# Optimization experiments

Hardware: AMD Instinct MI355X
Metric: run time of the kernel (lower is better)

## Reference

```python
import jax, jax.numpy as jnp
import numpy as np

def setup_inputs() -> dict:
    key = jax.random.key(0)
    k1, k2, k3 = jax.random.split(key, 3)
    B, N, D = 4, 2048, 1024
    x = jax.random.normal(k1, (B, N, D), dtype=jnp.float32)
    # nn.Linear weights are (out_features, in_features); init scale ~1/sqrt(D)
    W_Q = jax.random.normal(k2, (D, D), dtype=jnp.float32) / np.sqrt(D)
    W_K = jax.random.normal(k3, (D, D), dtype=jnp.float32) / np.sqrt(D)
    return {"x": x, "W_Q": W_Q, "W_K": W_K, "n_iters": 5}

def reference(x, W_Q, W_K, n_iters):
    # K = Linear(W_K)(x) = x @ W_K.T  -> (B, N, D)
    K = jnp.einsum('bnd,kd->bnk', x, W_K)
    y = x
    for _ in range(n_iters):
        Q = jnp.einsum('bnd,kd->bnk', y, W_Q)          # (B, N, D)
        scores = jnp.einsum('bnd,bmd->bnm', K, Q)       # K @ Q^T, (B, N, N)
        probs = jax.nn.softmax(scores, axis=-1)
        y = jnp.einsum('bnm,bmd->bnd', probs, x)        # (B, N, D)
    return y
```

## Files before the change

### kernel.cpp

```cpp
#include <hip/hip_runtime.h>
#include <cstdint>

typedef _Float16 f16;
typedef __attribute__((ext_vector_type(8))) _Float16 v8h;
typedef __attribute__((ext_vector_type(4))) float v4f;

#define LO_SCALE 4096.0f
#define LO_INV   2.44140625e-4f

__device__ __forceinline__ void split2(float f, f16& h, f16& l) {
    h = (f16)f;
    l = (f16)((f - (float)h) * LO_SCALE);
}

__device__ __forceinline__ void gload_lds16(const void* g, void* l) {
    __builtin_amdgcn_global_load_lds(
        (const __attribute__((address_space(1))) unsigned int*)(uintptr_t)g,
        (__attribute__((address_space(3))) unsigned int*)(unsigned int)(uintptr_t)l,
        16, 0, 0);
}

__global__ __launch_bounds__(256)
void gemm_nt_2limb(const f16* __restrict__ A1, const f16* __restrict__ A2,
                   const f16* __restrict__ B1, const f16* __restrict__ B2,
                   float* __restrict__ C32, f16* __restrict__ Ch,
                   f16* __restrict__ Cl, int mode, int N, int K)
{
    __shared__ f16 lds[4 * 128 * 32];
    f16* lA1 = lds;
    f16* lA2 = lds + 128 * 32;
    f16* lB1 = lds + 2 * 128 * 32;
    f16* lB2 = lds + 3 * 128 * 32;

    const int tid  = threadIdx.x;
    const int lane = tid & 63;
    const int wave = tid >> 6;
    const int wm = wave >> 1, wn = wave & 1;
    const int fr = lane & 15, quad = lane >> 4;
    const int row0 = blockIdx.y * 128;
    const int col0 = blockIdx.x * 128;
    const int l4 = lane >> 2;
    const int c8 = (lane & 3) * 8;

    v4f accB[4][4], accS[4][4];
#pragma unroll
    for (int i = 0; i < 4; ++i)
#pragma unroll
        for (int j = 0; j < 4; ++j) {
            accB[i][j] = {0.f, 0.f, 0.f, 0.f};
            accS[i][j] = {0.f, 0.f, 0.f, 0.f};
        }

    for (int k0 = 0; k0 < K; k0 += 32) {
#pragma unroll
        for (int t = 0; t < 2; ++t) {
            const int slot = wave + 4 * t;
            const int r = slot * 16 + l4;
            const size_t ga = (size_t)(row0 + r) * K + (k0 + c8);
            const size_t gb = (size_t)(col0 + r) * K + (k0 + c8);
            const unsigned loff = slot * 1024;
            gload_lds16(A1 + ga, (char*)lA1 + loff);
            gload_lds16(A2 + ga, (char*)lA2 + loff);
            gload_lds16(B1 + gb, (char*)lB1 + loff);
            gload_lds16(B2 + gb, (char*)lB2 + loff);
        }
        __syncthreads();

        v8h a1[4], a2[4], b1[4], b2[4];
#pragma unroll
        for (int i = 0; i < 4; ++i) {
            const int off = (wm * 64 + i * 16 + fr) * 32 + quad * 8;
            a1[i] = *(const v8h*)&lA1[off];
            a2[i] = *(const v8h*)&lA2[off];
        }
#pragma unroll
        for (int j = 0; j < 4; ++j) {
            const int off = (wn * 64 + j * 16 + fr) * 32 + quad * 8;
            b1[j] = *(const v8h*)&lB1[off];
            b2[j] = *(const v8h*)&lB2[off];
        }
#pragma unroll
        for (int i = 0; i < 4; ++i)
#pragma unroll
            for (int j = 0; j < 4; ++j) {
                accB[i][j] = __builtin_amdgcn_mfma_f32_16x16x32_f16(a1[i], b1[j], accB[i][j], 0, 0, 0);
                accS[i][j] = __builtin_amdgcn_mfma_f32_16x16x32_f16(a2[i], b1[j], accS[i][j], 0, 0, 0);
                accS[i][j] = __builtin_amdgcn_mfma_f32_16x16x32_f16(a1[i], b2[j], accS[i][j], 0, 0, 0);
            }
        __syncthreads();
    }

#pragma unroll
    for (int i = 0; i < 4; ++i)
#pragma unroll
        for (int j = 0; j < 4; ++j) {
            const int row = row0 + wm * 64 + i * 16 + quad * 4;
            const int col = col0 + wn * 64 + j * 16 + fr;
#pragma unroll
            for (int r = 0; r < 4; ++r) {
                const float v = accB[i][j][r] + accS[i][j][r] * LO_INV;
                const size_t off = (size_t)(row + r) * N + col;
                if (mode == 0) {
                    C32[off] = v;
                } else if (mode == 1) {
                    f16 h, l; split2(v, h, l);
                    Ch[off] = h; Cl[off] = l;
                } else {
                    C32[off] = v;
                    Ch[off] = (f16)v;
                }
            }
        }
}

__global__ __launch_bounds__(512)
void gemm_nt_2limb_256(const f16* __restrict__ A1, const f16* __restrict__ A2,
                       const f16* __restrict__ B1, const f16* __restrict__ B2,
                       float* __restrict__ C32, f16* __restrict__ Ch,
                       int N, int K)
{
    __shared__ f16 lds[2 * 24576];

    const int bid = blockIdx.x;
    const int lid = (bid & 7) * 32 + (bid >> 3);
    const int col0 = (lid & 7) * 128;
    const int row0 = (lid >> 3) * 256;

    const int tid  = threadIdx.x;
    const int lane = tid & 63;
    const int wave = tid >> 6;
    const int wm = wave >> 1;
    const int wn = wave & 1;
    const int fr = lane & 15, quad = lane >> 4;
    const int NT = K >> 5;

    const int trow = tid >> 2;
    const int tchunk = tid & 3;

    auto STAGE = [&](int T) {
        const unsigned bufB = (unsigned)(T & 1) * 49152u;
        const int k0 = T * 32;
#pragma unroll
        for (int rd = 0; rd < 2; ++rd) {
            const int r = trow + rd * 128;
            const int sc = (tchunk ^ ((r >> 1) & 3)) * 8;
            const size_t ga = (size_t)(row0 + r) * K + k0 + sc;
            const unsigned dof = (unsigned)(rd * 8192 + wave * 1024);
            gload_lds16(A1 + ga, (char*)lds + bufB + dof);
            gload_lds16(A2 + ga, (char*)lds + bufB + 16384u + dof);
        }
        {
            const int r = trow;
            const int sc = (tchunk ^ ((r >> 1) & 3)) * 8;
            const size_t gb = (size_t)(col0 + r) * K + k0 + sc;
            const unsigned dof = (unsigned)(wave * 1024);
            gload_lds16(B1 + gb, (char*)lds + bufB + 32768u + dof);
            gload_lds16(B2 + gb, (char*)lds + bufB + 40960u + dof);
        }
    };

    auto LRD = [&](const f16* base, int row) {
        return *(const v8h*)&base[row * 32 + ((quad ^ ((row >> 1) & 3)) * 8)];
    };

    v4f accB[4][4], accS[4][4];
#pragma unroll
    for (int i = 0; i < 4; ++i)
#pragma unroll
        for (int j = 0; j < 4; ++j) {
            accB[i][j] = {0.f, 0.f, 0.f, 0.f};
            accS[i][j] = {0.f, 0.f, 0.f, 0.f};
        }

    STAGE(0);
    asm volatile("s_waitcnt vmcnt(0)" ::: "memory");
    __builtin_amdgcn_s_barrier();

    for (int t = 0; t < NT; ++t) {
        const int bc = (t & 1) * 24576;
        const f16* lA1 = lds + bc;
        const f16* lA2 = lds + bc + 8192;
        const f16* lB1 = lds + bc + 16384;
        const f16* lB2 = lds + bc + 20480;

        v8h b1[4], b2[4];
#pragma unroll
        for (int j = 0; j < 4; ++j) {
            b1[j] = LRD(lB1, wn * 64 + j * 16 + fr);
            b2[j] = LRD(lB2, wn * 64 + j * 16 + fr);
        }
        {
            v8h a1 = LRD(lA1, wm * 64 + 0 + fr);
            v8h a2 = LRD(lA2, wm * 64 + 0 + fr);
            if (t + 1 < NT) STAGE(t + 1);
            __builtin_amdgcn_s_barrier();
            asm volatile("s_waitcnt lgkmcnt(0)" ::: "memory");
            __builtin_amdgcn_s_setprio(1);
#pragma unroll
            for (int j = 0; j < 4; ++j) {
                accB[0][j] = __builtin_amdgcn_mfma_f32_16x16x32_f16(a1, b1[j], accB[0][j], 0, 0, 0);
                accS[0][j] = __builtin_amdgcn_mfma_f32_16x16x32_f16(a2, b1[j], accS[0][j], 0, 0, 0);
                accS[0][j] = __builtin_amdgcn_mfma_f32_16x16x32_f16(a1, b2[j], accS[0][j], 0, 0, 0);
            }
            __builtin_amdgcn_s_setprio(0);
            __builtin_amdgcn_s_barrier();
        }

#pragma unroll
        for (int p = 1; p < 4; ++p) {
            v8h a1 = LRD(lA1, wm * 64 + p * 16 + fr);
            v8h a2 = LRD(lA2, wm * 64 + p * 16 + fr);
            __builtin_amdgcn_s_barrier();
            asm volatile("s_waitcnt lgkmcnt(0)" ::: "memory");
            __builtin_amdgcn_s_setprio(1);
#pragma unroll
            for (int j = 0; j < 4; ++j) {
                accB[p][j] = __builtin_amdgcn_mfma_f32_16x16x32_f16(a1, b1[j], accB[p][j], 0, 0, 0);
                accS[p][j] = __builtin_amdgcn_mfma_f32_16x16x32_f16(a2, b1[j], accS[p][j], 0, 0, 0);
                accS[p][j] = __builtin_amdgcn_mfma_f32_16x16x32_f16(a1, b2[j], accS[p][j], 0, 0, 0);
            }
            __builtin_amdgcn_s_setprio(0);
            if (p == 3)
                asm volatile("s_waitcnt vmcnt(0)" ::: "memory");
            __builtin_amdgcn_s_barrier();
        }
    }

#pragma unroll
    for (int i = 0; i < 4; ++i)
#pragma unroll
        for (int j = 0; j < 4; ++j) {
            const int row = row0 + wm * 64 + i * 16 + quad * 4;
            const int col = col0 + wn * 64 + j * 16 + fr;
#pragma unroll
            for (int r = 0; r < 4; ++r) {
                const float v = accB[i][j][r] + accS[i][j][r] * LO_INV;
                const size_t off = (size_t)(row + r) * N + col;
                C32[off] = v;
                Ch[off] = (f16)v;
            }
        }
}

__global__ __launch_bounds__(512)
void gemm_nt_f16_256(const f16* __restrict__ A, const f16* __restrict__ B,
                     f16* __restrict__ C, int N, int K,
                     size_t sA, size_t sB, size_t sC)
{
    __shared__ f16 lds[2 * 2 * 256 * 64];

    const int bz = blockIdx.z;
    A += (size_t)bz * sA; B += (size_t)bz * sB; C += (size_t)bz * sC;

    const int tid  = threadIdx.x;
    const int lane = tid & 63;
    const int wave = tid >> 6;
    const int wm = wave >> 2;
    const int wn = wave & 3;
    const int fr = lane & 15, quad = lane >> 4;
    const int row0 = blockIdx.y * 256;
    const int col0 = blockIdx.x * 256;
    const int NT = K >> 6;

    const int rsub = tid >> 3;
    const int csub = (((tid & 7) ^ ((tid >> 3) & 7)) * 8);

    auto STAGE = [&](int T) {
        const unsigned bufB = (unsigned)(T & 1) * 65536u;
#pragma unroll
        for (int q = 0; q < 4; ++q) {
            const f16* op = (q >= 2) ? B : A;
            const int r0 = ((q >= 2) ? col0 : row0) + (q & 1) * 128;
#pragma unroll
            for (int t2 = 0; t2 < 2; ++t2) {
                const f16* g = op + (size_t)(r0 + t2 * 64 + rsub) * K + T * 64 + csub;
                gload_lds16(g, (char*)lds + bufB + (unsigned)(q >> 1) * 32768u
                                 + (unsigned)(q & 1) * 16384u
                                 + (unsigned)(t2 * 8192 + wave * 1024));
            }
        }
    };

    auto LRD = [&](const f16* base, int row, int ks) {
        return *(const v8h*)&base[row * 64 + (((ks * 4 + quad) ^ (row & 7)) * 8)];
    };

    v4f acc[8][4];
#pragma unroll
    for (int i = 0; i < 8; ++i)
#pragma unroll
        for (int j = 0; j < 4; ++j)
            acc[i][j] = {0.f, 0.f, 0.f, 0.f};

    STAGE(0);
    asm volatile("s_waitcnt vmcnt(0)" ::: "memory");
    __builtin_amdgcn_s_barrier();

    for (int t = 0; t < NT; ++t) {
        const int bc = (t & 1) * 32768;
        const f16* lA = lds + bc;
        const f16* lB = lds + bc + 16384;

        v8h bfr[4][2];
#pragma unroll
        for (int j = 0; j < 4; ++j)
#pragma unroll
            for (int ks = 0; ks < 2; ++ks)
                bfr[j][ks] = LRD(lB, wn * 64 + j * 16 + fr, ks);
        {
            v8h a0[2], a1[2];
#pragma unroll
            for (int ks = 0; ks < 2; ++ks) {
                a0[ks] = LRD(lA, wm * 128 + 0 + fr, ks);
                a1[ks] = LRD(lA, wm * 128 + 16 + fr, ks);
            }
            if (t + 1 < NT) STAGE(t + 1);
            __builtin_amdgcn_s_barrier();
            asm volatile("s_waitcnt lgkmcnt(0)" ::: "memory");
            __builtin_amdgcn_s_setprio(1);
#pragma unroll
            for (int j = 0; j < 4; ++j) {
                acc[0][j] = __builtin_amdgcn_mfma_f32_16x16x32_f16(a0[0], bfr[j][0], acc[0][j], 0, 0, 0);
                acc[0][j] = __builtin_amdgcn_mfma_f32_16x16x32_f16(a0[1], bfr[j][1], acc[0][j], 0, 0, 0);
                acc[1][j] = __builtin_amdgcn_mfma_f32_16x16x32_f16(a1[0], bfr[j][0], acc[1][j], 0, 0, 0);
                acc[1][j] = __builtin_amdgcn_mfma_f32_16x16x32_f16(a1[1], bfr[j][1], acc[1][j], 0, 0, 0);
            }
            __builtin_amdgcn_s_setprio(0);
            __builtin_amdgcn_s_barrier();
        }

#pragma unroll
        for (int p = 1; p < 4; ++p) {
            v8h ap[2][2];
#pragma unroll
            for (int u = 0; u < 2; ++u)
#pragma unroll
                for (int ks = 0; ks < 2; ++ks)
                    ap[u][ks] = LRD(lA, wm * 128 + (p * 2 + u) * 16 + fr, ks);
            __builtin_amdgcn_s_barrier();
            asm volatile("s_waitcnt lgkmcnt(0)" ::: "memory");
            __builtin_amdgcn_s_setprio(1);
#pragma unroll
            for (int u = 0; u < 2; ++u)
#pragma unroll
                for (int j = 0; j < 4; ++j) {
                    acc[p * 2 + u][j] = __builtin_amdgcn_mfma_f32_16x16x32_f16(ap[u][0], bfr[j][0], acc[p * 2 + u][j], 0, 0, 0);
                    acc[p * 2 + u][j] = __builtin_amdgcn_mfma_f32_16x16x32_f16(ap[u][1], bfr[j][1], acc[p * 2 + u][j], 0, 0, 0);
                }
            __builtin_amdgcn_s_setprio(0);
            if (p == 3)
                asm volatile("s_waitcnt vmcnt(0)" ::: "memory");
            __builtin_amdgcn_s_barrier();
        }
    }

#pragma unroll
    for (int i = 0; i < 8; ++i)
#pragma unroll
        for (int j = 0; j < 4; ++j) {
            const int row = row0 + wm * 128 + i * 16 + quad * 4;
            const int col = col0 + wn * 64 + j * 16 + fr;
#pragma unroll
            for (int r = 0; r < 4; ++r)
                C[(size_t)(row + r) * N + col] = (f16)acc[i][j][r];
        }
}

__global__ __launch_bounds__(256)
void split_f32(const float* __restrict__ in, f16* __restrict__ h,
               f16* __restrict__ l, int n)
{
    const int i = (blockIdx.x * 256 + threadIdx.x) * 4;
    if (i >= n) return;
    const float4 v = *(const float4*)(in + i);
    f16 hh[4], ll[4];
    split2(v.x, hh[0], ll[0]);
    split2(v.y, hh[1], ll[1]);
    split2(v.z, hh[2], ll[2]);
    split2(v.w, hh[3], ll[3]);
    *(ushort4*)(h + i) = *(const ushort4*)hh;
    *(ushort4*)(l + i) = *(const ushort4*)ll;
}

__global__ __launch_bounds__(256)
void transpose_split(const float* __restrict__ in, f16* __restrict__ oh,
                     f16* __restrict__ ol, int R, int C)
{
    __shared__ float tile[32][33];
    const int tx = threadIdx.x & 31, ty = threadIdx.x >> 5;
    const int ic = blockIdx.x * 32 + tx;
    const int ir = blockIdx.y * 32 + ty;
#pragma unroll
    for (int k = 0; k < 32; k += 8)
        tile[ty + k][tx] = in[(size_t)(ir + k) * C + ic];
    __syncthreads();
    const int oc  = blockIdx.y * 32 + tx;
    const int orr = blockIdx.x * 32 + ty;
#pragma unroll
    for (int k = 0; k < 32; k += 8) {
        f16 h, l;
        split2(tile[tx][ty + k], h, l);
        oh[(size_t)(orr + k) * R + oc] = h;
        ol[(size_t)(orr + k) * R + oc] = l;
    }
}

#define CAP 1024

__global__ __launch_bounds__(256)
void refine_pv(const f16* __restrict__ S, const float* __restrict__ Kt,
               const float* __restrict__ Y, const float* __restrict__ X,
               float* __restrict__ Yout, f16* __restrict__ Yh)
{
    const int r = blockIdx.x;
    const int b = r >> 11;
    const int t = threadIdx.x;
    const int wave = t >> 6, lane = t & 63;

    __shared__ float red[4];
    __shared__ int cnt;
    __shared__ int idxs[CAP + 8];
    __shared__ float ex[CAP + 8];

    float s[8];
    {
        const v8h sv = *(const v8h*)(S + (size_t)r * 2048 + t * 8);
#pragma unroll
        for (int k = 0; k < 8; ++k) s[k] = (float)sv[k];
    }
    float m = s[0];
#pragma unroll
    for (int k = 1; k < 8; ++k) m = fmaxf(m, s[k]);
#pragma unroll
    for (int off = 32; off > 0; off >>= 1) m = fmaxf(m, __shfl_xor(m, off));
    if (lane == 0) red[wave] = m;
    if (t == 0) cnt = 0;
    __syncthreads();
    m = fmaxf(fmaxf(red[0], red[1]), fmaxf(red[2], red[3]));

    const float thresh = m - 18.0f;
#pragma unroll
    for (int k = 0; k < 8; ++k)
        if (s[k] > thresh) {
            const int p = atomicAdd(&cnt, 1);
            if (p < CAP) idxs[p] = t * 8 + k;
        }
    __syncthreads();
    const int count = min(cnt, CAP);

    const float* krow  = Kt + (size_t)r * 1024;
    const float* ybase = Y + (size_t)b * 2048 * 1024;
    for (int j = wave; j < count; j += 4) {
        const float* yrow = ybase + (size_t)idxs[j] * 1024;
        float acc = 0.f;
#pragma unroll
        for (int d = 0; d < 4; ++d) {
            const int e = lane * 4 + d * 256;
            const float4 kv = *(const float4*)(krow + e);
            const float4 yv = *(const float4*)(yrow + e);
            acc += kv.x * yv.x + kv.y * yv.y + kv.z * yv.z + kv.w * yv.w;
        }
#pragma unroll
        for (int off = 32; off > 0; off >>= 1) acc += __shfl_xor(acc, off);
        if (lane == 0) ex[j] = acc;
    }
    __syncthreads();

    float lm = -3.0e38f;
    for (int j = t; j < count; j += 256) lm = fmaxf(lm, ex[j]);
#pragma unroll
    for (int off = 32; off > 0; off >>= 1) lm = fmaxf(lm, __shfl_xor(lm, off));
    if (lane == 0) red[wave] = lm;
    __syncthreads();
    const float M2 = fmaxf(fmaxf(red[0], red[1]), fmaxf(red[2], red[3]));
    __syncthreads();

    float ls = 0.f;
    for (int j = t; j < count; j += 256) {
        const float e = expf(ex[j] - M2);
        ex[j] = e;
        ls += e;
    }
#pragma unroll
    for (int off = 32; off > 0; off >>= 1) ls += __shfl_xor(ls, off);
    if (lane == 0) red[wave] = ls;
    __syncthreads();
    const float inv = 1.0f / (red[0] + red[1] + red[2] + red[3]);
    for (int j = t; j < count; j += 256) ex[j] *= inv;
    const int countPad = (count + 7) & ~7;
    if (t < countPad - count) {
        ex[count + t]   = 0.f;
        idxs[count + t] = 0;
    }
    __syncthreads();

    const float* xb = X + (size_t)b * 2048 * 1024;
    float4 acc = {0.f, 0.f, 0.f, 0.f};
    for (int j = 0; j < countPad; j += 8) {
        float4 v[8];
        float  pw[8];
#pragma unroll
        for (int k = 0; k < 8; ++k) {
            pw[k] = ex[j + k];
            v[k] = *(const float4*)(xb + (size_t)idxs[j + k] * 1024 + t * 4);
        }
#pragma unroll
        for (int k = 0; k < 8; ++k) {
            acc.x += pw[k] * v[k].x;
            acc.y += pw[k] * v[k].y;
            acc.z += pw[k] * v[k].z;
            acc.w += pw[k] * v[k].w;
        }
    }
    const size_t o = (size_t)r * 1024 + t * 4;
    *(float4*)(Yout + o) = acc;
    f16 h[4] = {(f16)acc.x, (f16)acc.y, (f16)acc.z, (f16)acc.w};
    *(ushort4*)(Yh + o) = *(const ushort4*)h;
}

extern "C" void kernel_launch(void* const* d_in, const int* in_sizes, int n_in,
                              void* d_out, int out_size, void* d_ws, size_t ws_size,
                              hipStream_t stream)
{
    const float* x  = (const float*)d_in[0];
    const float* Wq = (const float*)d_in[1];
    const float* Wk = (const float*)d_in[2];
    const int n_iters = 5;

    const size_t NXe = 8388608;
    const size_t NWe = 1048576;
    const size_t NSe = 16777216;
    const size_t NR  = 8192;

    char* p = (char*)d_ws;
    f16* xh   = (f16*)p; p += NXe * 2;
    f16* xl   = (f16*)p; p += NXe * 2;
    f16* wkth = (f16*)p; p += NWe * 2;
    f16* wktl = (f16*)p; p += NWe * 2;
    f16* wqth = (f16*)p; p += NWe * 2;
    f16* wqtl = (f16*)p; p += NWe * 2;
    f16* vth  = (f16*)p; p += NWe * 2;
    f16* vtl  = (f16*)p; p += NWe * 2;
    float* kt32 = (float*)p; p += NXe * 4;
    f16*  kt16  = (f16*)p;  p += NXe * 2;
    f16*  st    = (f16*)p;  p += NSe * 2;
    f16*  yh    = (f16*)p;  p += NXe * 2;
    float* y1   = (float*)p; p += NXe * 4;
    float* y2   = (float*)p; p += NXe * 4;
    if ((size_t)(p - (char*)d_ws) > ws_size) return;

    float* out = (float*)d_out;

    split_f32<<<dim3(NXe / 1024), dim3(256), 0, stream>>>(x, xh, xl, (int)NXe);
    transpose_split<<<dim3(32, 32), dim3(256), 0, stream>>>(Wk, wkth, wktl, 1024, 1024);
    transpose_split<<<dim3(32, 32), dim3(256), 0, stream>>>(Wq, wqth, wqtl, 1024, 1024);
    gemm_nt_2limb<<<dim3(8, 8), dim3(256), 0, stream>>>(
        wqth, wqtl, wkth, wktl, nullptr, vth, vtl, 1, 1024, 1024);
    gemm_nt_2limb_256<<<dim3(256), dim3(512), 0, stream>>>(
        xh, xl, vth, vtl, kt32, kt16, 1024, 1024);

    const float* yr = x;
    float* pingpong[2] = {y1, y2};
    for (int it = 0; it < n_iters; ++it) {
        float* yw = (it == n_iters - 1) ? out : pingpong[it & 1];
        const f16* Bop = (it == 0) ? xh : yh;
        gemm_nt_f16_256<<<dim3(8, 8, 4), dim3(512), 0, stream>>>(
            kt16, Bop, st, 2048, 1024,
            (size_t)2048 * 1024, (size_t)2048 * 1024, (size_t)2048 * 2048);
        refine_pv<<<dim3(NR), dim3(256), 0, stream>>>(
            st, kt32, yr, x, yw, yh);
        yr = yw;
    }
}
```

Measured before the change: 729.0 us.

## Fuse refine scoring and PV accumulation with per-wave online softmax

Each wave now computes the refined score for a candidate row and immediately adds the matching X row into register accumulators, using an online-softmax running max and sum. The per-wave partial results are merged through shared memory at the end. This removes the separate max, exp and normalise passes and the extra block barriers, and keeps the K row in registers instead of reloading it for every candidate. In exchange it adds 16KB of shared memory per block, a cross-wave reduction, and possible rescale work whenever the running max changes.

```diff
diff --git a/kernel.cpp b/kernel.cpp
--- a/kernel.cpp
+++ b/kernel.cpp
@@ -418,9 +418,16 @@
     const int wave = t >> 6, lane = t & 63;
 
     __shared__ float red[4];
+    __shared__ float wmax[4], wsum[4];
     __shared__ int cnt;
-    __shared__ int idxs[CAP + 8];
-    __shared__ float ex[CAP + 8];
+    __shared__ int idxs[CAP];
+    __shared__ float accL[4][1024];
+
+    const float* krow = Kt + (size_t)r * 1024;
+    float4 kf[4];
+#pragma unroll
+    for (int d = 0; d < 4; ++d)
+        kf[d] = *(const float4*)(krow + d * 256 + lane * 4);
 
     float s[8];
     {
@@ -448,74 +455,75 @@
     __syncthreads();
     const int count = min(cnt, CAP);
 
-    const float* krow  = Kt + (size_t)r * 1024;
-    const float* ybase = Y + (size_t)b * 2048 * 1024;
+    const float* ybase = Y + ((size_t)b << 21);
+    const float* xbase = X + ((size_t)b << 21);
+    float m_run = m;
+    float sum = 0.f;
+    float4 acc[4];
+#pragma unroll
+    for (int d = 0; d < 4; ++d) acc[d] = {0.f, 0.f, 0.f, 0.f};
+
     for (int j = wave; j < count; j += 4) {
-        const float* yrow = ybase + (size_t)idxs[j] * 1024;
-        float acc = 0.f;
+        const int idx = idxs[j];
+        const float* yrow = ybase + (size_t)idx * 1024;
+        float e = 0.f;
 #pragma unroll
         for (int d = 0; d < 4; ++d) {
-            const int e = lane * 4 + d * 256;
-            const float4 kv = *(const float4*)(krow + e);
-            const float4 yv = *(const float4*)(yrow + e);
-            acc += kv.x * yv.x + kv.y * yv.y + kv.z * yv.z + kv.w * yv.w;
-        }
-#pragma unroll
-        for (int off = 32; off > 0; off >>= 1) acc += __shfl_xor(acc, off);
-        if (lane == 0) ex[j] = acc;
-    }
+            const float4 yv = *(const float4*)(yrow + d * 256 + lane * 4);
+            e += kf[d].x * yv.x + kf[d].y * yv.y + kf[d].z * yv.z + kf[d].w * yv.w;
+        }
+#pragma unroll
+        for (int off = 32; off > 0; off >>= 1) e += __shfl_xor(e, off);
+        if (e > m_run) {
+            const float sc = expf(m_run - e);
+            sum *= sc;
+#pragma unroll
+            for (int d = 0; d < 4; ++d) {
+                acc[d].x *= sc; acc[d].y *= sc; acc[d].z *= sc; acc[d].w *= sc;
+            }
+            m_run = e;
+        }
+        const float w = expf(e - m_run);
+        sum += w;
+        const float* xrow = xbase + (size_t)idx * 1024;
+#pragma unroll
+        for (int d = 0; d < 4; ++d) {
+            const float4 xv = *(const float4*)(xrow + d * 256 + lane * 4);
+            acc[d].x += w * xv.x; acc[d].y += w * xv.y;
+            acc[d].z += w * xv.z; acc[d].w += w * xv.w;
+        }
+    }
+
+    if (lane == 0) { wmax[wave] = m_run; wsum[wave] = sum; }
     __syncthreads();
-
-    float lm = -3.0e38f;
-    for (int j = t; j < count; j += 256) lm = fmaxf(lm, ex[j]);
-#pragma unroll
-    for (int off = 32; off > 0; off >>= 1) lm = fmaxf(lm, __shfl_xor(lm, off));
-    if (lane == 0) red[wave] = lm;
+    const float M = fmaxf(fmaxf(wmax[0], wmax[1]), fmaxf(wmax[2], wmax[3]));
+    float Stot = 0.f;
+#pragma unroll
+    for (int v = 0; v < 4; ++v) Stot += wsum[v] * expf(wmax[v] - M);
+    const float scale = expf(m_run - M) / Stot;
+#pragma unroll
+    for (int d = 0; d < 4; ++d) {
+        const int e0 = d * 256 + lane * 4;
+        float4 a = acc[d];
+        a.x *= scale; a.y *= scale; a.z *= scale; a.w *= scale;
+        *(float4*)&accL[wave][e0] = a;
+    }
     __syncthreads();
-    const float M2 = fmaxf(fmaxf(red[0], red[1]), fmaxf(red[2], red[3]));
-    __syncthreads();
-
-    float ls = 0.f;
-    for (int j = t; j < count; j += 256) {
-        const float e = expf(ex[j] - M2);
-        ex[j] = e;
-        ls += e;
-    }
-#pragma unroll
-    for (int off = 32; off > 0; off >>= 1) ls += __shfl_xor(ls, off);
-    if (lane == 0) red[wave] = ls;
-    __syncthreads();
-    const float inv = 1.0f / (red[0] + red[1] + red[2] + red[3]);
-    for (int j = t; j < count; j += 256) ex[j] *= inv;
-    const int countPad = (count + 7) & ~7;
-    if (t < countPad - count) {
-        ex[count + t]   = 0.f;
-        idxs[count + t] = 0;
-    }
-    __syncthreads();
-
-    const float* xb = X + (size_t)b * 2048 * 1024;
-    float4 acc = {0.f, 0.f, 0.f, 0.f};
-    for (int j = 0; j < countPad; j += 8) {
-        float4 v[8];
-        float  pw[8];
-#pragma unroll
-        for (int k = 0; k < 8; ++k) {
-            pw[k] = ex[j + k];
-            v[k] = *(const float4*)(xb + (size_t)idxs[j + k] * 1024 + t * 4);
-        }
-#pragma unroll
-        for (int k = 0; k < 8; ++k) {
-            acc.x += pw[k] * v[k].x;
-            acc.y += pw[k] * v[k].y;
-            acc.z += pw[k] * v[k].z;
-            acc.w += pw[k] * v[k].w;
-        }
-    }
-    const size_t o = (size_t)r * 1024 + t * 4;
-    *(float4*)(Yout + o) = acc;
-    f16 h[4] = {(f16)acc.x, (f16)acc.y, (f16)acc.z, (f16)acc.w};
-    *(ushort4*)(Yh + o) = *(const ushort4*)h;
+
+    const int e0 = t * 4;
+    float4 o = *(const float4*)&accL[0][e0];
+    const float4 o1 = *(const float4*)&accL[1][e0];
+    const float4 o2 = *(const float4*)&accL[2][e0];
+    const float4 o3 = *(const float4*)&accL[3][e0];
+    o.x += o1.x + o2.x + o3.x;
+    o.y += o1.y + o2.y + o3.y;
+    o.z += o1.z + o2.z + o3.z;
+    o.w += o1.w + o2.w + o3.w;
+
+    const size_t oo = (size_t)r * 1024 + e0;
+    *(float4*)(Yout + oo) = o;
+    f16 h[4] = {(f16)o.x, (f16)o.y, (f16)o.z, (f16)o.w};
+    *(ushort4*)(Yh + oo) = *(const ushort4*)h;
 }
 
 extern "C" void kernel_launch(void* const* d_in, const int* in_sizes, int n_in,
```

Result: no change. 716.4 us (-1.7%).
